# Kernel tuning notes

Hardware: AMD Instinct MI355X
Metric: run time of the kernel (lower is better)

## Reference

```python
import jax, jax.numpy as jnp
import numpy as np

EPS = 1e-12
N, C, B = 8, 2048, 2048


def setup_inputs() -> dict:
    key = jax.random.key(0)
    kx, kk, kq = jax.random.split(key, 3)
    # Xavier-uniform bound for [C,C] weight
    bound = float(np.sqrt(6.0 / (C + C)))
    X = jax.random.normal(kx, (N, C, B), dtype=jnp.float32)
    Wk = jax.random.uniform(kk, (C, C), minval=-bound, maxval=bound, dtype=jnp.float32)
    Wq = jax.random.uniform(kq, (C, C), minval=-bound, maxval=bound, dtype=jnp.float32)
    Wk0 = jnp.zeros((C, 1), dtype=jnp.float32)
    Wq0 = jnp.zeros((C, 1), dtype=jnp.float32)
    return {"X": X, "Wk": Wk, "Wq": Wq, "Wk0": Wk0, "Wq0": Wq0}


def reference(X, Wk, Wq, Wk0, Wq0):
    # X: [N,C,B]; Wk,Wq: [C,C]; Wk0,Wq0: [C,1] (broadcast over B)
    K = jnp.einsum('ij,njb->nib', Wk, X) + Wk0  # [N,C,B]
    Q = jnp.einsum('ij,njb->nib', Wq, X) + Wq0  # [N,C,B]
    DK2 = jnp.sum(K * K, axis=2)  # [N,C] squared row norms
    DQ2 = jnp.sum(Q * Q, axis=2)  # [N,C]
    DQK = jnp.sqrt(jnp.maximum(DQ2[:, :, None] * DK2[:, None, :], EPS))  # [N,C,C]
    Y = jnp.einsum('nib,njb->nij', Q, K) / DQK  # cosine-normalized scores [N,C,C]
    SM = jax.nn.softmax(Y, axis=1)  # softmax over query-channel axis
    # Z = (X^T @ SM)^T : Z[n,j,b] = sum_c X[n,c,b] * SM[n,c,j]
    Z = jnp.einsum('ncb,ncj->njb', X, SM)  # [N,C,B]
    return Z
```

## Files before the change

kernel.cpp:

```cpp
#include <hip/hip_runtime.h>
#include <hip/hip_bf16.h>

typedef __bf16 bf16_t;
typedef __bf16 bf16x8 __attribute__((ext_vector_type(8)));
typedef __bf16 bf16x4 __attribute__((ext_vector_type(4)));
typedef float  f32x4  __attribute__((ext_vector_type(4)));

#define NB 8
#define CD 2048
#define BD 2048
#define LD 2048
#define BK 64
#define NT (LD / BK)

#define BAR()    asm volatile("s_barrier" ::: "memory")
#define WAITL0() asm volatile("s_waitcnt lgkmcnt(0)" ::: "memory")
#define WAITV(n) asm volatile("s_waitcnt vmcnt(" #n ")" ::: "memory")

__global__ void k_transpose_x(const float* __restrict__ X, bf16_t* __restrict__ XbT) {
    __shared__ bf16_t tile[64][66];
    const int t = threadIdx.x;
    const int b0 = blockIdx.x * 64, c0 = blockIdx.y * 64, n = blockIdx.z;
    const float* Xn = X + (size_t)n * CD * BD;
    bf16_t* Tn = XbT + (size_t)n * BD * CD;
    const int cl = t & 63, rw = t >> 6;
#pragma unroll
    for (int r = 0; r < 16; ++r) {
        int row = r * 4 + rw;
        tile[row][cl] = (bf16_t)Xn[(size_t)(c0 + row) * BD + b0 + cl];
    }
    __syncthreads();
#pragma unroll
    for (int r = 0; r < 16; ++r) {
        int row = r * 4 + rw;
        Tn[(size_t)(b0 + row) * CD + c0 + cl] = tile[cl][row];
    }
}

__global__ void k_convert_w(const float* __restrict__ Wk, const float* __restrict__ Wq,
                            bf16_t* __restrict__ Wkb, bf16_t* __restrict__ Wqb) {
    const size_t i = ((size_t)blockIdx.x * 256 + threadIdx.x) * 4;
    const float* src = blockIdx.y ? Wq : Wk;
    bf16_t* dst = blockIdx.y ? Wqb : Wkb;
    float4 v = *(const float4*)(src + i);
    bf16x4 o;
    o[0] = (bf16_t)v.x; o[1] = (bf16_t)v.y; o[2] = (bf16_t)v.z; o[3] = (bf16_t)v.w;
    *(bf16x4*)(dst + i) = o;
}


__device__ __forceinline__ void gll16(const bf16_t* g, bf16_t* l) {
    __builtin_amdgcn_global_load_lds((const __attribute__((address_space(1))) void*)g,
                                     (__attribute__((address_space(3))) void*)l, 16, 0, 0);
}

__device__ __forceinline__ void stage_half(const bf16_t* gsrc, bf16_t* ldsh, int w, int l) {
    const int rr = l >> 3;
    const int ce = ((l & 7) ^ rr) * 8;
#pragma unroll
    for (int i = 0; i < 2; ++i) {
        const bf16_t* g = gsrc + (size_t)(i * 64 + w * 8 + rr) * LD + ce;
        gll16(g, ldsh + i * 4096 + w * 512);
    }
}

__device__ __forceinline__ bf16x8 lds_frag(const bf16_t* hbase, int row16, int lr, int st, int ks, int swz) {
    const int r = row16 + lr;
    const int ce = (st * 32 + ks * 8) ^ swz;
    return *(const bf16x8*)(hbase + r * 64 + ce);
}

template <int EPI>
__global__ __launch_bounds__(512, 2) void k_gemm256(const bf16_t* __restrict__ Aall, size_t sA,
                                                    const bf16_t* __restrict__ Ball, size_t sB,
                                                    void* __restrict__ Call, size_t sC,
                                                    const float* __restrict__ bias) {
    __shared__ alignas(16) bf16_t Ah[2][2][128 * 64];
    __shared__ alignas(16) bf16_t Bh[2][2][128 * 64];
    const int tid = threadIdx.x;
    const int lane = tid & 63, wave = tid >> 6;
    const int wm = wave >> 2, wn = wave & 3;
    const int lr = lane & 15, ks = lane >> 4;
    const int swz = (lr & 7) << 3;

    const int bid = blockIdx.x;
    const int lin = (bid & 7) * 64 + (bid >> 3);
    const int z = lin >> 6, rem = lin & 63, bm = rem >> 3, bn = rem & 7;
    const int m0 = bm * 256, n0 = bn * 256;

    const bf16_t* Ab = Aall + sA * z + (size_t)m0 * LD;
    const bf16_t* Bb = Ball + sB * z + (size_t)n0 * LD;

    stage_half(Ab,                &Ah[0][0][0], wave, lane);
    stage_half(Bb,                &Bh[0][0][0], wave, lane);
    stage_half(Ab + 128 * LD,     &Ah[0][1][0], wave, lane);
    stage_half(Bb + 128 * LD,     &Bh[0][1][0], wave, lane);
    stage_half(Ab + BK,           &Ah[1][0][0], wave, lane);
    stage_half(Bb + BK,           &Bh[1][0][0], wave, lane);
    WAITV(8); BAR();

    f32x4 acc[8][4] = {};
    bf16x8 af[4][2], b0[2][2], b1[2][2];

    for (int t = 0; t < NT; ++t) {
        const int cur = t & 1, nxt = cur ^ 1;
        const int t1 = (t + 1 < NT) ? t + 1 : NT - 1;
        const int t2 = (t + 2 < NT) ? t + 2 : NT - 1;
        const bf16_t* A0c = &Ah[cur][0][0];
        const bf16_t* A1c = &Ah[cur][1][0];
        const bf16_t* B0c = &Bh[cur][0][0];
        const bf16_t* B1c = &Bh[cur][1][0];

#pragma unroll
        for (int s = 0; s < 4; ++s)
#pragma unroll
            for (int st = 0; st < 2; ++st)
                af[s][st] = lds_frag(A0c, (s * 2 + wm) * 16, lr, st, ks, swz);
#pragma unroll
        for (int u = 0; u < 2; ++u)
#pragma unroll
            for (int st = 0; st < 2; ++st)
                b0[u][st] = lds_frag(B0c, (u * 4 + wn) * 16, lr, st, ks, swz);
        stage_half(Ab + 128 * LD + t1 * BK, &Ah[nxt][1][0], wave, lane);
        WAITV(6); BAR(); WAITL0();
        __builtin_amdgcn_s_setprio(1);
#pragma unroll
        for (int s = 0; s < 4; ++s)
#pragma unroll
            for (int u = 0; u < 2; ++u)
#pragma unroll
                for (int st = 0; st < 2; ++st)
                    acc[s][u] = __builtin_amdgcn_mfma_f32_16x16x32_bf16(af[s][st], b0[u][st], acc[s][u], 0, 0, 0);
        __builtin_amdgcn_s_setprio(0);
        BAR();

#pragma unroll
        for (int u = 0; u < 2; ++u)
#pragma unroll
            for (int st = 0; st < 2; ++st)
                b1[u][st] = lds_frag(B1c, (u * 4 + wn) * 16, lr, st, ks, swz);
        stage_half(Bb + 128 * LD + t1 * BK, &Bh[nxt][1][0], wave, lane);
        BAR(); WAITL0();
        __builtin_amdgcn_s_setprio(1);
#pragma unroll
        for (int s = 0; s < 4; ++s)
#pragma unroll
            for (int u = 0; u < 2; ++u)
#pragma unroll
                for (int st = 0; st < 2; ++st)
                    acc[s][2 + u] = __builtin_amdgcn_mfma_f32_16x16x32_bf16(af[s][st], b1[u][st], acc[s][2 + u], 0, 0, 0);
        __builtin_amdgcn_s_setprio(0);
        BAR();

#pragma unroll
        for (int s = 0; s < 4; ++s)
#pragma unroll
            for (int st = 0; st < 2; ++st)
                af[s][st] = lds_frag(A1c, (s * 2 + wm) * 16, lr, st, ks, swz);
        stage_half(Ab + t2 * BK, &Ah[cur][0][0], wave, lane);
        BAR(); WAITL0();
        __builtin_amdgcn_s_setprio(1);
#pragma unroll
        for (int s = 0; s < 4; ++s)
#pragma unroll
            for (int u = 0; u < 2; ++u)
#pragma unroll
                for (int st = 0; st < 2; ++st)
                    acc[4 + s][u] = __builtin_amdgcn_mfma_f32_16x16x32_bf16(af[s][st], b0[u][st], acc[4 + s][u], 0, 0, 0);
        __builtin_amdgcn_s_setprio(0);
        BAR();

        stage_half(Bb + t2 * BK, &Bh[cur][0][0], wave, lane);
        WAITV(8); BAR();
        __builtin_amdgcn_s_setprio(1);
#pragma unroll
        for (int s = 0; s < 4; ++s)
#pragma unroll
            for (int u = 0; u < 2; ++u)
#pragma unroll
                for (int st = 0; st < 2; ++st)
                    acc[4 + s][2 + u] = __builtin_amdgcn_mfma_f32_16x16x32_bf16(af[s][st], b1[u][st], acc[4 + s][2 + u], 0, 0, 0);
        __builtin_amdgcn_s_setprio(0);
        BAR();
    }
    WAITV(0);

    const int rsub = ks * 4;
#pragma unroll
    for (int f = 0; f < 8; ++f) {
        const int h = f >> 2, s = f & 3;
        const int rb = m0 + h * 128 + (s * 2 + wm) * 16 + rsub;
#pragma unroll
        for (int j = 0; j < 4; ++j) {
            const int r = rb + j;
            float bv = 0.f;
            if (EPI == 1) bv = bias[r];
#pragma unroll
            for (int g = 0; g < 4; ++g) {
                const int c = n0 + (g >> 1) * 128 + ((g & 1) * 4 + wn) * 16 + lr;
                const float v = acc[f][g][j] + bv;
                if (EPI == 1) ((bf16_t*)Call)[sC * z + (size_t)r * LD + c] = (bf16_t)v;
                else          ((float*)Call)[sC * z + (size_t)r * LD + c] = v;
            }
        }
    }
}

__global__ void k_row_norm2(const bf16_t* __restrict__ Kb, const bf16_t* __restrict__ Qb,
                            float* __restrict__ DK2, float* __restrict__ DQ2) {
    const int row = blockIdx.x, n = blockIdx.y;
    const bf16_t* src = blockIdx.z ? Qb : Kb;
    float* dst = blockIdx.z ? DQ2 : DK2;
    const bf16_t* pr = src + ((size_t)n * CD + row) * BD + threadIdx.x * 8;
    bf16x8 v = *(const bf16x8*)pr;
    float s = 0.f;
#pragma unroll
    for (int e = 0; e < 8; ++e) { float x = (float)v[e]; s += x * x; }
#pragma unroll
    for (int off = 32; off; off >>= 1) s += __shfl_xor(s, off, 64);
    __shared__ float ws[4];
    if ((threadIdx.x & 63) == 0) ws[threadIdx.x >> 6] = s;
    __syncthreads();
    if (threadIdx.x == 0) dst[(size_t)n * CD + row] = ws[0] + ws[1] + ws[2] + ws[3];
}

__global__ void k_softmax_rows(const float* __restrict__ Yt, const float* __restrict__ DK2,
                               const float* __restrict__ DQ2, bf16_t* __restrict__ SMT) {
    const int j = blockIdx.x, n = blockIdx.y, t = threadIdx.x;
    const int lane = t & 63, wave = t >> 6;
    const float* y = Yt + ((size_t)n * CD + j) * CD;
    const float* q2 = DQ2 + (size_t)n * CD;
    const float dk2 = DK2[(size_t)n * CD + j];
    const int i0 = t * 8;

    float v[8];
    float4 a = *(const float4*)(y + i0);
    float4 b = *(const float4*)(y + i0 + 4);
    float4 qa = *(const float4*)(q2 + i0);
    float4 qb = *(const float4*)(q2 + i0 + 4);
    v[0] = a.x * rsqrtf(fmaxf(dk2 * qa.x, 1e-12f));
    v[1] = a.y * rsqrtf(fmaxf(dk2 * qa.y, 1e-12f));
    v[2] = a.z * rsqrtf(fmaxf(dk2 * qa.z, 1e-12f));
    v[3] = a.w * rsqrtf(fmaxf(dk2 * qa.w, 1e-12f));
    v[4] = b.x * rsqrtf(fmaxf(dk2 * qb.x, 1e-12f));
    v[5] = b.y * rsqrtf(fmaxf(dk2 * qb.y, 1e-12f));
    v[6] = b.z * rsqrtf(fmaxf(dk2 * qb.z, 1e-12f));
    v[7] = b.w * rsqrtf(fmaxf(dk2 * qb.w, 1e-12f));

    float m = v[0];
#pragma unroll
    for (int e = 1; e < 8; ++e) m = fmaxf(m, v[e]);
#pragma unroll
    for (int off = 32; off; off >>= 1) m = fmaxf(m, __shfl_xor(m, off, 64));
    __shared__ float redm[4], reds[4];
    if (lane == 0) redm[wave] = m;
    __syncthreads();
    m = fmaxf(fmaxf(redm[0], redm[1]), fmaxf(redm[2], redm[3]));

    float e8[8];
    float s = 0.f;
#pragma unroll
    for (int e = 0; e < 8; ++e) { e8[e] = __expf(v[e] - m); s += e8[e]; }
#pragma unroll
    for (int off = 32; off; off >>= 1) s += __shfl_xor(s, off, 64);
    if (lane == 0) reds[wave] = s;
    __syncthreads();
    s = reds[0] + reds[1] + reds[2] + reds[3];
    const float inv = 1.f / s;

    bf16x8 o;
#pragma unroll
    for (int e = 0; e < 8; ++e) o[e] = (bf16_t)(e8[e] * inv);
    *(bf16x8*)(SMT + ((size_t)n * CD + j) * CD + i0) = o;
}

extern "C" void kernel_launch(void* const* d_in, const int* in_sizes, int n_in,
                              void* d_out, int out_size, void* d_ws, size_t ws_size,
                              hipStream_t stream) {
    const float* X   = (const float*)d_in[0];
    const float* Wk  = (const float*)d_in[1];
    const float* Wq  = (const float*)d_in[2];
    const float* Wk0 = (const float*)d_in[3];
    const float* Wq0 = (const float*)d_in[4];
    float* Z = (float*)d_out;

    const size_t NCB = (size_t)NB * CD * BD;
    const size_t CC  = (size_t)CD * CD;
    const size_t NCC = (size_t)NB * CC;

    char* p = (char*)d_ws;
    bf16_t* XbT = (bf16_t*)p; p += NCB * 2;
    bf16_t* Wkb = (bf16_t*)p; p += CC * 2;
    bf16_t* Wqb = (bf16_t*)p; p += CC * 2;
    bf16_t* Kb  = (bf16_t*)p; p += NCB * 2;
    bf16_t* Qb  = (bf16_t*)p; p += NCB * 2;
    float*  DK2 = (float*)p;  p += (size_t)NB * CD * 4;
    float*  DQ2 = (float*)p;  p += (size_t)NB * CD * 4;
    float*  Yt  = (float*)p;  p += NCC * 4;
    bf16_t* SMT = Kb;
    if ((size_t)(p - (char*)d_ws) > ws_size) return;

    dim3 blk(256);
    k_transpose_x<<<dim3(BD / 64, CD / 64, NB), blk, 0, stream>>>(X, XbT);
    k_convert_w<<<dim3(CC / 1024, 2), blk, 0, stream>>>(Wk, Wq, Wkb, Wqb);
    k_gemm256<1><<<512, 512, 0, stream>>>(Wkb, 0, XbT, (size_t)BD * CD, Kb, (size_t)CD * BD, Wk0);
    k_gemm256<1><<<512, 512, 0, stream>>>(Wqb, 0, XbT, (size_t)BD * CD, Qb, (size_t)CD * BD, Wq0);
    k_row_norm2<<<dim3(CD, NB, 2), blk, 0, stream>>>(Kb, Qb, DK2, DQ2);
    k_gemm256<0><<<512, 512, 0, stream>>>(Kb, (size_t)CD * BD, Qb, (size_t)CD * BD, Yt, CC, nullptr);
    k_softmax_rows<<<dim3(CD, NB), blk, 0, stream>>>(Yt, DK2, DQ2, SMT);
    k_gemm256<0><<<512, 512, 0, stream>>>(SMT, CC, XbT, (size_t)BD * CD, Z, (size_t)CD * BD, nullptr);
}
```

Before: 658.6 us.

## Software-pipeline LDS fragment loads one phase ahead of MFMA in batched GEMM

Restructures the GEMM main loop so each phase loads the register fragments needed by the next MFMA block while the current MFMAs run. The A0/B0 fragments for the next k-tile are prefetched at the end of the iteration, and the explicit lgkmcnt(0) waits and one barrier per phase are removed. This is meant to hide LDS read latency behind matrix math and cut synchronisation stalls. The cost is more live fragment registers (separate A0/A1/B0/B1 sets) and relying on compiler-inserted waits, with revised vmcnt counts that could be subtly wrong.

```diff
diff --git a/kernel.cpp b/kernel.cpp
--- a/kernel.cpp
+++ b/kernel.cpp
@@ -14,7 +14,6 @@
 #define NT (LD / BK)
 
 #define BAR()    asm volatile("s_barrier" ::: "memory")
-#define WAITL0() asm volatile("s_waitcnt lgkmcnt(0)" ::: "memory")
 #define WAITV(n) asm volatile("s_waitcnt vmcnt(" #n ")" ::: "memory")
 
 __global__ void k_transpose_x(const float* __restrict__ X, bf16_t* __restrict__ XbT) {
@@ -91,38 +90,99 @@
     const bf16_t* Ab = Aall + sA * z + (size_t)m0 * LD;
     const bf16_t* Bb = Ball + sB * z + (size_t)n0 * LD;
 
-    stage_half(Ab,                &Ah[0][0][0], wave, lane);
-    stage_half(Bb,                &Bh[0][0][0], wave, lane);
-    stage_half(Ab + 128 * LD,     &Ah[0][1][0], wave, lane);
-    stage_half(Bb + 128 * LD,     &Bh[0][1][0], wave, lane);
-    stage_half(Ab + BK,           &Ah[1][0][0], wave, lane);
-    stage_half(Bb + BK,           &Bh[1][0][0], wave, lane);
-    WAITV(8); BAR();
+    stage_half(Ab,            &Ah[0][0][0], wave, lane);
+    stage_half(Bb,            &Bh[0][0][0], wave, lane);
+    stage_half(Ab + 128 * LD, &Ah[0][1][0], wave, lane);
+    stage_half(Bb + 128 * LD, &Bh[0][1][0], wave, lane);
+    stage_half(Ab + BK,       &Ah[1][0][0], wave, lane);
+    stage_half(Bb + BK,       &Bh[1][0][0], wave, lane);
+    WAITV(8);
+    BAR();
 
     f32x4 acc[8][4] = {};
-    bf16x8 af[4][2], b0[2][2], b1[2][2];
+    bf16x8 fA0[4][2], fA1[4][2], fB0[2][2], fB1[2][2];
+
+#pragma unroll
+    for (int s = 0; s < 4; ++s)
+#pragma unroll
+        for (int st = 0; st < 2; ++st)
+            fA0[s][st] = lds_frag(&Ah[0][0][0], (s * 2 + wm) * 16, lr, st, ks, swz);
+#pragma unroll
+    for (int u = 0; u < 2; ++u)
+#pragma unroll
+        for (int st = 0; st < 2; ++st)
+            fB0[u][st] = lds_frag(&Bh[0][0][0], (u * 4 + wn) * 16, lr, st, ks, swz);
 
     for (int t = 0; t < NT; ++t) {
         const int cur = t & 1, nxt = cur ^ 1;
         const int t1 = (t + 1 < NT) ? t + 1 : NT - 1;
         const int t2 = (t + 2 < NT) ? t + 2 : NT - 1;
-        const bf16_t* A0c = &Ah[cur][0][0];
         const bf16_t* A1c = &Ah[cur][1][0];
-        const bf16_t* B0c = &Bh[cur][0][0];
         const bf16_t* B1c = &Bh[cur][1][0];
-
-#pragma unroll
-        for (int s = 0; s < 4; ++s)
+        const bf16_t* A0n = &Ah[nxt][0][0];
+        const bf16_t* B0n = &Bh[nxt][0][0];
+
+        BAR();
+        WAITV(4);
+#pragma unroll
+        for (int u = 0; u < 2; ++u)
 #pragma unroll
             for (int st = 0; st < 2; ++st)
-                af[s][st] = lds_frag(A0c, (s * 2 + wm) * 16, lr, st, ks, swz);
+                fB1[u][st] = lds_frag(B1c, (u * 4 + wn) * 16, lr, st, ks, swz);
+        stage_half(Ab + 128 * LD + t1 * BK, &Ah[nxt][1][0], wave, lane);
+        __builtin_amdgcn_s_setprio(1);
+#pragma unroll
+        for (int s = 0; s < 4; ++s)
+#pragma unroll
+            for (int u = 0; u < 2; ++u)
+#pragma unroll
+                for (int st = 0; st < 2; ++st)
+                    acc[s][u] = __builtin_amdgcn_mfma_f32_16x16x32_bf16(fA0[s][st], fB0[u][st], acc[s][u], 0, 0, 0);
+        __builtin_amdgcn_s_setprio(0);
+
+        BAR();
+#pragma unroll
+        for (int s = 0; s < 4; ++s)
+#pragma unroll
+            for (int st = 0; st < 2; ++st)
+                fA1[s][st] = lds_frag(A1c, (s * 2 + wm) * 16, lr, st, ks, swz);
+        stage_half(Bb + 128 * LD + t1 * BK, &Bh[nxt][1][0], wave, lane);
+        __builtin_amdgcn_s_setprio(1);
+#pragma unroll
+        for (int s = 0; s < 4; ++s)
+#pragma unroll
+            for (int u = 0; u < 2; ++u)
+#pragma unroll
+                for (int st = 0; st < 2; ++st)
+                    acc[s][2 + u] = __builtin_amdgcn_mfma_f32_16x16x32_bf16(fA0[s][st], fB1[u][st], acc[s][2 + u], 0, 0, 0);
+        __builtin_amdgcn_s_setprio(0);
+
+        BAR();
+        WAITV(6);
+#pragma unroll
+        for (int s = 0; s < 4; ++s)
+#pragma unroll
+            for (int st = 0; st < 2; ++st)
+                fA0[s][st] = lds_frag(A0n, (s * 2 + wm) * 16, lr, st, ks, swz);
+        stage_half(Ab + t2 * BK, &Ah[cur][0][0], wave, lane);
+        __builtin_amdgcn_s_setprio(1);
+#pragma unroll
+        for (int s = 0; s < 4; ++s)
+#pragma unroll
+            for (int u = 0; u < 2; ++u)
+#pragma unroll
+                for (int st = 0; st < 2; ++st)
+                    acc[4 + s][u] = __builtin_amdgcn_mfma_f32_16x16x32_bf16(fA1[s][st], fB0[u][st], acc[4 + s][u], 0, 0, 0);
+        __builtin_amdgcn_s_setprio(0);
+
+        BAR();
+        WAITV(6);
 #pragma unroll
         for (int u = 0; u < 2; ++u)
 #pragma unroll
             for (int st = 0; st < 2; ++st)
-                b0[u][st] = lds_frag(B0c, (u * 4 + wn) * 16, lr, st, ks, swz);
-        stage_half(Ab + 128 * LD + t1 * BK, &Ah[nxt][1][0], wave, lane);
-        WAITV(6); BAR(); WAITL0();
+                fB0[u][st] = lds_frag(B0n, (u * 4 + wn) * 16, lr, st, ks, swz);
+        stage_half(Bb + t2 * BK, &Bh[cur][0][0], wave, lane);
         __builtin_amdgcn_s_setprio(1);
 #pragma unroll
         for (int s = 0; s < 4; ++s)
@@ -130,58 +190,8 @@
             for (int u = 0; u < 2; ++u)
 #pragma unroll
                 for (int st = 0; st < 2; ++st)
-                    acc[s][u] = __builtin_amdgcn_mfma_f32_16x16x32_bf16(af[s][st], b0[u][st], acc[s][u], 0, 0, 0);
+                    acc[4 + s][2 + u] = __builtin_amdgcn_mfma_f32_16x16x32_bf16(fA1[s][st], fB1[u][st], acc[4 + s][2 + u], 0, 0, 0);
         __builtin_amdgcn_s_setprio(0);
-        BAR();
-
-#pragma unroll
-        for (int u = 0; u < 2; ++u)
-#pragma unroll
-            for (int st = 0; st < 2; ++st)
-                b1[u][st] = lds_frag(B1c, (u * 4 + wn) * 16, lr, st, ks, swz);
-        stage_half(Bb + 128 * LD + t1 * BK, &Bh[nxt][1][0], wave, lane);
-        BAR(); WAITL0();
-        __builtin_amdgcn_s_setprio(1);
-#pragma unroll
-        for (int s = 0; s < 4; ++s)
-#pragma unroll
-            for (int u = 0; u < 2; ++u)
-#pragma unroll
-                for (int st = 0; st < 2; ++st)
-                    acc[s][2 + u] = __builtin_amdgcn_mfma_f32_16x16x32_bf16(af[s][st], b1[u][st], acc[s][2 + u], 0, 0, 0);
-        __builtin_amdgcn_s_setprio(0);
-        BAR();
-
-#pragma unroll
-        for (int s = 0; s < 4; ++s)
-#pragma unroll
-            for (int st = 0; st < 2; ++st)
-                af[s][st] = lds_frag(A1c, (s * 2 + wm) * 16, lr, st, ks, swz);
-        stage_half(Ab + t2 * BK, &Ah[cur][0][0], wave, lane);
-        BAR(); WAITL0();
-        __builtin_amdgcn_s_setprio(1);
-#pragma unroll
-        for (int s = 0; s < 4; ++s)
-#pragma unroll
-            for (int u = 0; u < 2; ++u)
-#pragma unroll
-                for (int st = 0; st < 2; ++st)
-                    acc[4 + s][u] = __builtin_amdgcn_mfma_f32_16x16x32_bf16(af[s][st], b0[u][st], acc[4 + s][u], 0, 0, 0);
-        __builtin_amdgcn_s_setprio(0);
-        BAR();
-
-        stage_half(Bb + t2 * BK, &Bh[cur][0][0], wave, lane);
-        WAITV(8); BAR();
-        __builtin_amdgcn_s_setprio(1);
-#pragma unroll
-        for (int s = 0; s < 4; ++s)
-#pragma unroll
-            for (int u = 0; u < 2; ++u)
-#pragma unroll
-                for (int st = 0; st < 2; ++st)
-                    acc[4 + s][2 + u] = __builtin_amdgcn_mfma_f32_16x16x32_bf16(af[s][st], b1[u][st], acc[4 + s][2 + u], 0, 0, 0);
-        __builtin_amdgcn_s_setprio(0);
-        BAR();
     }
     WAITV(0);
 
```

Result: faster. 627.0 us (-4.8%).

## Unroll GEMM main loop by two K-tiles and restructure LDS prefetch schedule

Applied to the files above, without the earlier changes.

Rewrites the 256x256 bf16 MFMA GEMM main loop to process two K-tiles per iteration with fixed buffer slots, so the double-buffer indices are compile-time constants. It changes the wave-to-fragment mapping: each wave now owns contiguous 64-row and 32-column blocks instead of interleaved 16-row strips. It also adds partial lgkmcnt waits and reorders the global-to-LDS staging so the prefetch of the next tiles overlaps more with the MFMA work. The aim is to cut address arithmetic and barrier stalls, at the cost of larger code and a more fragile hand-written wait-count schedule.

```diff
diff --git a/kernel.cpp b/kernel.cpp
--- a/kernel.cpp
+++ b/kernel.cpp
@@ -12,9 +12,11 @@
 #define LD 2048
 #define BK 64
 #define NT (LD / BK)
+#define NP (NT / 2)
 
 #define BAR()    asm volatile("s_barrier" ::: "memory")
 #define WAITL0() asm volatile("s_waitcnt lgkmcnt(0)" ::: "memory")
+#define WAITL8() asm volatile("s_waitcnt lgkmcnt(8)" ::: "memory")
 #define WAITV(n) asm volatile("s_waitcnt vmcnt(" #n ")" ::: "memory")
 
 __global__ void k_transpose_x(const float* __restrict__ X, bf16_t* __restrict__ XbT) {
@@ -75,8 +77,8 @@
                                                     const bf16_t* __restrict__ Ball, size_t sB,
                                                     void* __restrict__ Call, size_t sC,
                                                     const float* __restrict__ bias) {
-    __shared__ alignas(16) bf16_t Ah[2][2][128 * 64];
-    __shared__ alignas(16) bf16_t Bh[2][2][128 * 64];
+    __shared__ alignas(16) bf16_t As[2][2][128 * 64];
+    __shared__ alignas(16) bf16_t Bs[2][2][128 * 64];
     const int tid = threadIdx.x;
     const int lane = tid & 63, wave = tid >> 6;
     const int wm = wave >> 2, wn = wave & 3;
@@ -91,119 +93,124 @@
     const bf16_t* Ab = Aall + sA * z + (size_t)m0 * LD;
     const bf16_t* Bb = Ball + sB * z + (size_t)n0 * LD;
 
-    stage_half(Ab,                &Ah[0][0][0], wave, lane);
-    stage_half(Bb,                &Bh[0][0][0], wave, lane);
-    stage_half(Ab + 128 * LD,     &Ah[0][1][0], wave, lane);
-    stage_half(Bb + 128 * LD,     &Bh[0][1][0], wave, lane);
-    stage_half(Ab + BK,           &Ah[1][0][0], wave, lane);
-    stage_half(Bb + BK,           &Bh[1][0][0], wave, lane);
-    WAITV(8); BAR();
-
-    f32x4 acc[8][4] = {};
-    bf16x8 af[4][2], b0[2][2], b1[2][2];
-
-    for (int t = 0; t < NT; ++t) {
-        const int cur = t & 1, nxt = cur ^ 1;
-        const int t1 = (t + 1 < NT) ? t + 1 : NT - 1;
-        const int t2 = (t + 2 < NT) ? t + 2 : NT - 1;
-        const bf16_t* A0c = &Ah[cur][0][0];
-        const bf16_t* A1c = &Ah[cur][1][0];
-        const bf16_t* B0c = &Bh[cur][0][0];
-        const bf16_t* B1c = &Bh[cur][1][0];
-
-#pragma unroll
-        for (int s = 0; s < 4; ++s)
+    stage_half(Ab,                 &As[0][0][0], wave, lane);
+    stage_half(Bb,                 &Bs[0][0][0], wave, lane);
+    stage_half(Ab + 128 * LD,      &As[0][1][0], wave, lane);
+    stage_half(Bb + 128 * LD,      &Bs[0][1][0], wave, lane);
+    WAITV(4);
+    stage_half(Ab + BK,            &As[1][0][0], wave, lane);
+    stage_half(Bb + BK,            &Bs[1][0][0], wave, lane);
+    stage_half(Bb + 128 * LD + BK, &Bs[1][1][0], wave, lane);
+    WAITV(6);
+    BAR();
+
+    f32x4 acc[2][2][4][2] = {};
+    bf16x8 afr[4][2], bf0[2][2], bf1[2][2];
+
+    auto RD_A = [&](int slot, int half) {
+#pragma unroll
+        for (int mi = 0; mi < 4; ++mi)
 #pragma unroll
             for (int st = 0; st < 2; ++st)
-                af[s][st] = lds_frag(A0c, (s * 2 + wm) * 16, lr, st, ks, swz);
-#pragma unroll
-        for (int u = 0; u < 2; ++u)
+                afr[mi][st] = lds_frag(&As[slot][half][0], wm * 64 + mi * 16, lr, st, ks, swz);
+    };
+    auto RD_B = [&](bf16x8 (&dst)[2][2], int slot, int half) {
+#pragma unroll
+        for (int ni = 0; ni < 2; ++ni)
 #pragma unroll
             for (int st = 0; st < 2; ++st)
-                b0[u][st] = lds_frag(B0c, (u * 4 + wn) * 16, lr, st, ks, swz);
-        stage_half(Ab + 128 * LD + t1 * BK, &Ah[nxt][1][0], wave, lane);
-        WAITV(6); BAR(); WAITL0();
+                dst[ni][st] = lds_frag(&Bs[slot][half][0], wn * 32 + ni * 16, lr, st, ks, swz);
+    };
+    auto MFMA_Q = [&](int mh, int nh, bf16x8 (&bsrc)[2][2]) {
         __builtin_amdgcn_s_setprio(1);
 #pragma unroll
-        for (int s = 0; s < 4; ++s)
-#pragma unroll
-            for (int u = 0; u < 2; ++u)
+        for (int mi = 0; mi < 4; ++mi)
+#pragma unroll
+            for (int ni = 0; ni < 2; ++ni)
 #pragma unroll
                 for (int st = 0; st < 2; ++st)
-                    acc[s][u] = __builtin_amdgcn_mfma_f32_16x16x32_bf16(af[s][st], b0[u][st], acc[s][u], 0, 0, 0);
+                    acc[mh][nh][mi][ni] = __builtin_amdgcn_mfma_f32_16x16x32_bf16(
+                        afr[mi][st], bsrc[ni][st], acc[mh][nh][mi][ni], 0, 0, 0);
         __builtin_amdgcn_s_setprio(0);
-        BAR();
-
-#pragma unroll
-        for (int u = 0; u < 2; ++u)
-#pragma unroll
-            for (int st = 0; st < 2; ++st)
-                b1[u][st] = lds_frag(B1c, (u * 4 + wn) * 16, lr, st, ks, swz);
-        stage_half(Bb + 128 * LD + t1 * BK, &Bh[nxt][1][0], wave, lane);
-        BAR(); WAITL0();
-        __builtin_amdgcn_s_setprio(1);
-#pragma unroll
-        for (int s = 0; s < 4; ++s)
-#pragma unroll
-            for (int u = 0; u < 2; ++u)
-#pragma unroll
-                for (int st = 0; st < 2; ++st)
-                    acc[s][2 + u] = __builtin_amdgcn_mfma_f32_16x16x32_bf16(af[s][st], b1[u][st], acc[s][2 + u], 0, 0, 0);
-        __builtin_amdgcn_s_setprio(0);
-        BAR();
-
-#pragma unroll
-        for (int s = 0; s < 4; ++s)
-#pragma unroll
-            for (int st = 0; st < 2; ++st)
-                af[s][st] = lds_frag(A1c, (s * 2 + wm) * 16, lr, st, ks, swz);
-        stage_half(Ab + t2 * BK, &Ah[cur][0][0], wave, lane);
-        BAR(); WAITL0();
-        __builtin_amdgcn_s_setprio(1);
-#pragma unroll
-        for (int s = 0; s < 4; ++s)
-#pragma unroll
-            for (int u = 0; u < 2; ++u)
-#pragma unroll
-                for (int st = 0; st < 2; ++st)
-                    acc[4 + s][u] = __builtin_amdgcn_mfma_f32_16x16x32_bf16(af[s][st], b0[u][st], acc[4 + s][u], 0, 0, 0);
-        __builtin_amdgcn_s_setprio(0);
-        BAR();
-
-        stage_half(Bb + t2 * BK, &Bh[cur][0][0], wave, lane);
-        WAITV(8); BAR();
-        __builtin_amdgcn_s_setprio(1);
-#pragma unroll
-        for (int s = 0; s < 4; ++s)
-#pragma unroll
-            for (int u = 0; u < 2; ++u)
-#pragma unroll
-                for (int st = 0; st < 2; ++st)
-                    acc[4 + s][2 + u] = __builtin_amdgcn_mfma_f32_16x16x32_bf16(af[s][st], b1[u][st], acc[4 + s][2 + u], 0, 0, 0);
-        __builtin_amdgcn_s_setprio(0);
+    };
+
+    for (int tp = 0; tp < NP; ++tp) {
+        const int u = 2 * tp, v = u + 1;
+        const int w = (u + 2 < NT) ? u + 2 : NT - 1;
+        const int x = (v + 2 < NT) ? v + 2 : NT - 1;
+
+        RD_A(0, 0); RD_B(bf0, 0, 0);
+        stage_half(Ab + 128 * LD + v * BK, &As[1][1][0], wave, lane);
+        WAITL8();
+        BAR(); WAITL0();
+        MFMA_Q(0, 0, bf0);
+        BAR();
+
+        RD_B(bf1, 0, 1);
+        stage_half(Ab + w * BK, &As[0][0][0], wave, lane);
+        BAR(); WAITL0();
+        MFMA_Q(0, 1, bf1);
+        BAR();
+
+        RD_A(0, 1);
+        stage_half(Bb + w * BK, &Bs[0][0][0], wave, lane);
+        BAR(); WAITL0();
+        MFMA_Q(1, 0, bf0);
+        BAR();
+
+        stage_half(Bb + 128 * LD + w * BK, &Bs[0][1][0], wave, lane);
+        WAITV(6);
+        BAR();
+        MFMA_Q(1, 1, bf1);
+        BAR();
+
+        RD_A(1, 0); RD_B(bf0, 1, 0);
+        stage_half(Ab + 128 * LD + w * BK, &As[0][1][0], wave, lane);
+        WAITL8();
+        BAR(); WAITL0();
+        MFMA_Q(0, 0, bf0);
+        BAR();
+
+        RD_B(bf1, 1, 1);
+        stage_half(Ab + x * BK, &As[1][0][0], wave, lane);
+        BAR(); WAITL0();
+        MFMA_Q(0, 1, bf1);
+        BAR();
+
+        RD_A(1, 1);
+        stage_half(Bb + x * BK, &Bs[1][0][0], wave, lane);
+        BAR(); WAITL0();
+        MFMA_Q(1, 0, bf0);
+        BAR();
+
+        stage_half(Bb + 128 * LD + x * BK, &Bs[1][1][0], wave, lane);
+        WAITV(6);
+        BAR();
+        MFMA_Q(1, 1, bf1);
         BAR();
     }
     WAITV(0);
 
     const int rsub = ks * 4;
 #pragma unroll
-    for (int f = 0; f < 8; ++f) {
-        const int h = f >> 2, s = f & 3;
-        const int rb = m0 + h * 128 + (s * 2 + wm) * 16 + rsub;
-#pragma unroll
-        for (int j = 0; j < 4; ++j) {
-            const int r = rb + j;
-            float bv = 0.f;
-            if (EPI == 1) bv = bias[r];
-#pragma unroll
-            for (int g = 0; g < 4; ++g) {
-                const int c = n0 + (g >> 1) * 128 + ((g & 1) * 4 + wn) * 16 + lr;
-                const float v = acc[f][g][j] + bv;
-                if (EPI == 1) ((bf16_t*)Call)[sC * z + (size_t)r * LD + c] = (bf16_t)v;
-                else          ((float*)Call)[sC * z + (size_t)r * LD + c] = v;
+    for (int mh = 0; mh < 2; ++mh)
+#pragma unroll
+        for (int mi = 0; mi < 4; ++mi)
+#pragma unroll
+            for (int j = 0; j < 4; ++j) {
+                const int r = m0 + mh * 128 + wm * 64 + mi * 16 + rsub + j;
+                float bv = 0.f;
+                if (EPI == 1) bv = bias[r];
+#pragma unroll
+                for (int nh = 0; nh < 2; ++nh)
+#pragma unroll
+                    for (int ni = 0; ni < 2; ++ni) {
+                        const int c = n0 + nh * 128 + wn * 32 + ni * 16 + lr;
+                        const float vv = acc[mh][nh][mi][ni][j] + bv;
+                        if (EPI == 1) ((bf16_t*)Call)[sC * z + (size_t)r * LD + c] = (bf16_t)vv;
+                        else          ((float*)Call)[sC * z + (size_t)r * LD + c] = vv;
+                    }
             }
-        }
-    }
 }
 
 __global__ void k_row_norm2(const bf16_t* __restrict__ Kb, const bf16_t* __restrict__ Qb,
```

Result: faster. 607.0 us (-7.8%).
